# Performance work log

Hardware: AMD Instinct MI355X
Metric: run time of the kernel (lower is better)

The kernel has to match this reference:

```python
import jax, jax.numpy as jnp
import numpy as np
from jax import lax

D = 512
K = 5
HID = 2 * D
EPS = 1e-5


def layernorm(x, g, b):
    mu = jnp.mean(x, axis=-1, keepdims=True)
    var = jnp.mean((x - mu) ** 2, axis=-1, keepdims=True)
    return (x - mu) * lax.rsqrt(var + EPS) * g + b


def setup_inputs() -> dict:
    key = jax.random.key(0)
    ks = jax.random.split(key, 16)
    B, T = 8, 4096
    sc = lambda fan: 1.0 / np.sqrt(fan)
    return {
        "x": jax.random.normal(ks[0], (B, T, D), jnp.float32),
        "decay_logit": jnp.zeros((D,), jnp.float32),
        "W_out": jax.random.uniform(ks[1], (D, D), jnp.float32, -sc(D), sc(D)),
        "b_out": jax.random.uniform(ks[2], (D,), jnp.float32, -sc(D), sc(D)),
        "conv_w": jax.random.uniform(ks[3], (D, 1, K), jnp.float32, -sc(K), sc(K)),
        "conv_b": jax.random.uniform(ks[4], (D,), jnp.float32, -sc(K), sc(K)),
        "ln1_g": jnp.ones((D,), jnp.float32),
        "ln1_b": jnp.zeros((D,), jnp.float32),
        "ln2_g": jnp.ones((D,), jnp.float32),
        "ln2_b": jnp.zeros((D,), jnp.float32),
        "W1": jax.random.uniform(ks[5], (HID, D), jnp.float32, -sc(D), sc(D)),
        "b1": jax.random.uniform(ks[6], (HID,), jnp.float32, -sc(D), sc(D)),
        "W2": jax.random.uniform(ks[7], (D, HID), jnp.float32, -sc(HID), sc(HID)),
        "b2": jax.random.uniform(ks[8], (D,), jnp.float32, -sc(HID), sc(HID)),
    }


def retention_core(xn, decay_logit, W_out, b_out, conv_w, conv_b):
    # xn: [B, T, D]
    B, T, _ = xn.shape
    a = jax.nn.sigmoid(decay_logit)  # [D]

    def step(s, xt):  # s, xt: [B, D]
        s = a * s + (1.0 - a) * xt
        return s, s

    s0 = jnp.zeros((B, D), xn.dtype)
    _, ss = lax.scan(step, s0, jnp.swapaxes(xn, 0, 1))  # [T, B, D]
    ss = jnp.swapaxes(ss, 0, 1)  # [B, T, D]
    y_ret = jnp.einsum("btd,ed->bte", ss, W_out) + b_out

    # depthwise conv1d, 'same' padding (K odd)
    xc = jnp.swapaxes(xn, 1, 2)  # [B, D, T]
    pad = (K - 1) // 2
    y_loc = lax.conv_general_dilated(
        xc, conv_w, window_strides=(1,), padding=[(pad, pad)],
        feature_group_count=D, dimension_numbers=("NCH", "OIH", "NCH"))
    y_loc = jnp.swapaxes(y_loc + conv_b[None, :, None], 1, 2)  # [B, T, D]
    return y_ret + y_loc


def reference(x, decay_logit, W_out, b_out, conv_w, conv_b,
              ln1_g, ln1_b, ln2_g, ln2_b, W1, b1, W2, b2):
    y = retention_core(layernorm(x, ln1_g, ln1_b),
                       decay_logit, W_out, b_out, conv_w, conv_b)
    x = x + y
    h = layernorm(x, ln2_g, ln2_b)
    h = jax.nn.gelu(jnp.einsum("btd,hd->bth", h, W1) + b1, approximate=False)
    y = jnp.einsum("bth,dh->btd", h, W2) + b2
    return x + y
```

## Files before the change

kernel.cpp:

```cpp
#include <hip/hip_runtime.h>
#include <stdint.h>

typedef unsigned short u16;

#define DIM 512
#define HIDN 1024
#define TT 4096
#define BB 8
#define MM 32768
#define CH 128
#define CL 32

__device__ __forceinline__ u16 f2bf(float f) {
  union { float f; uint32_t u; } v; v.f = f;
  uint32_t u = v.u;
  uint32_t r = u + 0x7fffu + ((u >> 16) & 1u);
  return (u16)(r >> 16);
}
__device__ __forceinline__ float bf2f(u16 h) {
  union { uint32_t u; float f; } v; v.u = ((uint32_t)h) << 16; return v.f;
}

typedef __bf16 bf16x8 __attribute__((ext_vector_type(8)));
typedef float f32x4 __attribute__((ext_vector_type(4)));

__global__ __launch_bounds__(256) void prep_kernel(
    const float* __restrict__ wout, const float* __restrict__ w1,
    const float* __restrict__ w2, const float* __restrict__ dl,
    const float* __restrict__ convw,
    u16* __restrict__ wout_h, u16* __restrict__ w1_h, u16* __restrict__ w2_h,
    float* __restrict__ a, float* __restrict__ oma, float* __restrict__ aL,
    float* __restrict__ convwT) {
  int i = blockIdx.x * 256 + threadIdx.x;
  if (i < DIM * DIM) wout_h[i] = f2bf(wout[i]);
  if (i < HIDN * DIM) { w1_h[i] = f2bf(w1[i]); w2_h[i] = f2bf(w2[i]); }
  if (i < 5 * DIM) {
    int kk = i / DIM, n = i - kk * DIM;
    convwT[i] = convw[n * 5 + kk];
  }
  if (i < DIM) {
    float av = 1.0f / (1.0f + expf(-dl[i]));
    a[i] = av; oma[i] = 1.0f - av; aL[i] = powf(av, (float)CL);
  }
}

__global__ __launch_bounds__(256) void ln_rows(
    const float* __restrict__ xin, const float* __restrict__ g,
    const float* __restrict__ bvec, u16* __restrict__ out) {
  int lane = threadIdx.x & 63, wave = threadIdx.x >> 6;
  size_t row = (size_t)blockIdx.x * 4 + wave;
  const float4* xr = (const float4*)(xin + row * DIM);
  float4 v0 = xr[lane * 2 + 0];
  float4 v1 = xr[lane * 2 + 1];
  float s1 = v0.x + v0.y + v0.z + v0.w + v1.x + v1.y + v1.z + v1.w;
  float s2 = v0.x * v0.x + v0.y * v0.y + v0.z * v0.z + v0.w * v0.w
           + v1.x * v1.x + v1.y * v1.y + v1.z * v1.z + v1.w * v1.w;
#pragma unroll
  for (int o = 1; o < 64; o <<= 1) { s1 += __shfl_xor(s1, o); s2 += __shfl_xor(s2, o); }
  float mu = s1 * (1.0f / DIM);
  float var = s2 * (1.0f / DIM) - mu * mu;
  float rs = rsqrtf(var + 1e-5f);
  const float4* gr = (const float4*)g;
  const float4* br = (const float4*)bvec;
  float4 g0 = gr[lane * 2], g1 = gr[lane * 2 + 1];
  float4 b0 = br[lane * 2], b1 = br[lane * 2 + 1];
  uint32_t p0 = (uint32_t)f2bf((v0.x - mu) * rs * g0.x + b0.x) | ((uint32_t)f2bf((v0.y - mu) * rs * g0.y + b0.y) << 16);
  uint32_t p1 = (uint32_t)f2bf((v0.z - mu) * rs * g0.z + b0.z) | ((uint32_t)f2bf((v0.w - mu) * rs * g0.w + b0.w) << 16);
  uint32_t p2 = (uint32_t)f2bf((v1.x - mu) * rs * g1.x + b1.x) | ((uint32_t)f2bf((v1.y - mu) * rs * g1.y + b1.y) << 16);
  uint32_t p3 = (uint32_t)f2bf((v1.z - mu) * rs * g1.z + b1.z) | ((uint32_t)f2bf((v1.w - mu) * rs * g1.w + b1.w) << 16);
  uint4 pk; pk.x = p0; pk.y = p1; pk.z = p2; pk.w = p3;
  ((uint4*)(out + row * DIM))[lane] = pk;
}

__global__ __launch_bounds__(256) void scan_local(
    const u16* __restrict__ xn, const float* __restrict__ a,
    const float* __restrict__ oma, float* __restrict__ carry) {
  int idx = blockIdx.x * 256 + threadIdx.x;
  int dp = (idx & 255) * 2;
  int c = (idx >> 8) & (CH - 1);
  int b = idx >> 15;
  float a0 = a[dp], a1 = a[dp + 1], o0 = oma[dp], o1 = oma[dp + 1];
  const uint32_t* xp = (const uint32_t*)(xn + ((size_t)(b * TT + c * CL)) * DIM + dp);
  float s0 = 0.f, s1 = 0.f;
#pragma unroll
  for (int i = 0; i < CL; ++i) {
    uint32_t u = xp[(size_t)i * (DIM / 2)];
    s0 = fmaf(a0, s0, o0 * bf2f((u16)(u & 0xffffu)));
    s1 = fmaf(a1, s1, o1 * bf2f((u16)(u >> 16)));
  }
  float2 cv; cv.x = s0; cv.y = s1;
  *(float2*)&carry[((size_t)(b * CH + c)) * DIM + dp] = cv;
}

__global__ __launch_bounds__(256) void scan_carry(
    const float* __restrict__ carry, const float* __restrict__ aL,
    float* __restrict__ start) {
  int idx = blockIdx.x * 256 + threadIdx.x;
  int d = idx & (DIM - 1);
  int b = idx >> 9;
  float al = aL[d];
  float s = 0.f;
#pragma unroll 8
  for (int c = 0; c < CH; ++c) {
    size_t o = ((size_t)(b * CH + c)) * DIM + d;
    start[o] = s;
    s = fmaf(al, s, carry[o]);
  }
}

__global__ __launch_bounds__(256) void scan_emit(
    const u16* __restrict__ xn, const float* __restrict__ a,
    const float* __restrict__ oma, const float* __restrict__ start,
    u16* __restrict__ ss) {
  int idx = blockIdx.x * 256 + threadIdx.x;
  int dp = (idx & 255) * 2;
  int c = (idx >> 8) & (CH - 1);
  int b = idx >> 15;
  float a0 = a[dp], a1 = a[dp + 1], o0 = oma[dp], o1 = oma[dp + 1];
  const uint32_t* xp = (const uint32_t*)(xn + ((size_t)(b * TT + c * CL)) * DIM + dp);
  uint32_t* sp = (uint32_t*)(ss + ((size_t)(b * TT + c * CL)) * DIM + dp);
  float2 st = *(const float2*)&start[((size_t)(b * CH + c)) * DIM + dp];
  float s0 = st.x, s1 = st.y;
#pragma unroll
  for (int i = 0; i < CL; ++i) {
    uint32_t u = xp[(size_t)i * (DIM / 2)];
    s0 = fmaf(a0, s0, o0 * bf2f((u16)(u & 0xffffu)));
    s1 = fmaf(a1, s1, o1 * bf2f((u16)(u >> 16)));
    sp[(size_t)i * (DIM / 2)] = (uint32_t)f2bf(s0) | ((uint32_t)f2bf(s1) << 16);
  }
}

template <int Kd, int NCOL, int EPI>
__global__ __launch_bounds__(512, 4) void gemm_bt(
    const u16* __restrict__ A, const u16* __restrict__ Bmat,
    const float* __restrict__ bias, const float* __restrict__ resid,
    const u16* __restrict__ xn, const float* __restrict__ convwT,
    const float* __restrict__ convb, float* __restrict__ outf,
    u16* __restrict__ outh) {
  __shared__ alignas(16) u16 sA[2][128 * 64];
  __shared__ alignas(16) u16 sB[2][128 * 64];
  const int tid = threadIdx.x;
  const int lane = tid & 63, wave = tid >> 6;
  const int wm = wave >> 2;
  const int wn = wave & 3;
  const int rA = lane & 15, q = lane >> 4;

  const int lin = blockIdx.x;
  const int tile_col = (lin >> 3) & (NCOL - 1);
  const int tile_row = (lin & 7) + 8 * ((lin >> 3) / NCOL);
  const size_t rowTile = (size_t)tile_row * 128;
  const size_t colTile = (size_t)tile_col * 128;

  f32x4 acc[4][2];
#pragma unroll
  for (int i = 0; i < 4; i++)
#pragma unroll
    for (int j = 0; j < 2; j++) acc[i][j] = (f32x4){0.f, 0.f, 0.f, 0.f};

  const u16* Abase = A + rowTile * Kd;
  const u16* Bbase = Bmat + colTile * Kd;

  const int lrow = lane >> 3;
  const int lslot = lane & 7;
  const int gk = ((lslot ^ lrow) & 7) * 8;

  auto stage = [&](int kt, int buf) {
#pragma unroll
    for (int it = 0; it < 2; ++it) {
      const int m0 = (it * 8 + wave) * 8;
      const u16* ga = Abase + (size_t)(m0 + lrow) * Kd + kt + gk;
      const u16* gb = Bbase + (size_t)(m0 + lrow) * Kd + kt + gk;
      __builtin_amdgcn_global_load_lds(
          (const __attribute__((address_space(1))) void*)ga,
          (__attribute__((address_space(3))) void*)&sA[buf][m0 * 64], 16, 0, 0);
      __builtin_amdgcn_global_load_lds(
          (const __attribute__((address_space(1))) void*)gb,
          (__attribute__((address_space(3))) void*)&sB[buf][m0 * 64], 16, 0, 0);
    }
  };

  constexpr int NI = Kd / 64;
  stage(0, 0);
#pragma unroll 1
  for (int i = 0; i < NI; ++i) {
    __asm__ __volatile__("s_barrier" ::: "memory");
    if (i + 1 < NI) {
      stage((i + 1) * 64, (i + 1) & 1);
      __asm__ __volatile__("s_waitcnt vmcnt(4)" ::: "memory");
    } else {
      __asm__ __volatile__("s_waitcnt vmcnt(0)" ::: "memory");
    }
    __asm__ __volatile__("s_barrier" ::: "memory");
    const u16* bufA = sA[i & 1];
    const u16* bufB = sB[i & 1];
#pragma unroll
    for (int ks = 0; ks < 2; ++ks) {
      bf16x8 af[4], bfr[2];
#pragma unroll
      for (int mi = 0; mi < 4; ++mi) {
        int r = wm * 64 + mi * 16 + rA;
        int pos = ((ks * 4 + q) ^ (r & 7));
        af[mi] = *(const bf16x8*)&bufA[r * 64 + pos * 8];
      }
#pragma unroll
      for (int ni = 0; ni < 2; ++ni) {
        int r = wn * 32 + ni * 16 + rA;
        int pos = ((ks * 4 + q) ^ (r & 7));
        bfr[ni] = *(const bf16x8*)&bufB[r * 64 + pos * 8];
      }
#pragma unroll
      for (int mi = 0; mi < 4; ++mi)
#pragma unroll
        for (int ni = 0; ni < 2; ++ni)
          acc[mi][ni] = __builtin_amdgcn_mfma_f32_16x16x32_bf16(bfr[ni], af[mi], acc[mi][ni], 0, 0, 0);
    }
  }

#pragma unroll
  for (int mi = 0; mi < 4; ++mi) {
    size_t m = rowTile + wm * 64 + mi * 16 + rA;
#pragma unroll
    for (int ni = 0; ni < 2; ++ni) {
      int n0 = (int)colTile + wn * 32 + ni * 16 + q * 4;
      f32x4 v = acc[mi][ni];
      float4 bv = *(const float4*)&bias[n0];
      float val0 = v[0] + bv.x, val1 = v[1] + bv.y, val2 = v[2] + bv.z, val3 = v[3] + bv.w;
      if constexpr (EPI == 0) {
        int t = (int)(m & (TT - 1));
        float4 cb = *(const float4*)&convb[n0];
        float4 rv = *(const float4*)&resid[m * DIM + n0];
        val0 += cb.x + rv.x; val1 += cb.y + rv.y; val2 += cb.z + rv.z; val3 += cb.w + rv.w;
#pragma unroll
        for (int kk = 0; kk < 5; ++kk) {
          int ttc = t + kk - 2;
          if (ttc >= 0 && ttc < TT) {
            uint2 xv = *(const uint2*)&xn[(m + (size_t)kk - 2) * DIM + n0];
            float4 wv = *(const float4*)&convwT[kk * DIM + n0];
            val0 = fmaf(wv.x, bf2f((u16)(xv.x & 0xffffu)), val0);
            val1 = fmaf(wv.y, bf2f((u16)(xv.x >> 16)), val1);
            val2 = fmaf(wv.z, bf2f((u16)(xv.y & 0xffffu)), val2);
            val3 = fmaf(wv.w, bf2f((u16)(xv.y >> 16)), val3);
          }
        }
        float4 ov; ov.x = val0; ov.y = val1; ov.z = val2; ov.w = val3;
        *(float4*)&outf[m * DIM + n0] = ov;
      } else if constexpr (EPI == 1) {
        const float isq2 = 0.70710678118654752f;
        float g0 = 0.5f * val0 * (1.0f + erff(val0 * isq2));
        float g1 = 0.5f * val1 * (1.0f + erff(val1 * isq2));
        float g2 = 0.5f * val2 * (1.0f + erff(val2 * isq2));
        float g3 = 0.5f * val3 * (1.0f + erff(val3 * isq2));
        uint2 pk;
        pk.x = (uint32_t)f2bf(g0) | ((uint32_t)f2bf(g1) << 16);
        pk.y = (uint32_t)f2bf(g2) | ((uint32_t)f2bf(g3) << 16);
        *(uint2*)&outh[m * HIDN + n0] = pk;
      } else {
        float4 rv = *(const float4*)&resid[m * DIM + n0];
        float4 ov;
        ov.x = val0 + rv.x; ov.y = val1 + rv.y; ov.z = val2 + rv.z; ov.w = val3 + rv.w;
        *(float4*)&outf[m * DIM + n0] = ov;
      }
    }
  }
}

extern "C" void kernel_launch(void* const* d_in, const int* in_sizes, int n_in,
                              void* d_out, int out_size, void* d_ws, size_t ws_size,
                              hipStream_t stream) {
  const float* x      = (const float*)d_in[0];
  const float* dl     = (const float*)d_in[1];
  const float* W_out  = (const float*)d_in[2];
  const float* b_out  = (const float*)d_in[3];
  const float* conv_w = (const float*)d_in[4];
  const float* conv_b = (const float*)d_in[5];
  const float* ln1_g  = (const float*)d_in[6];
  const float* ln1_b  = (const float*)d_in[7];
  const float* ln2_g  = (const float*)d_in[8];
  const float* ln2_b  = (const float*)d_in[9];
  const float* W1     = (const float*)d_in[10];
  const float* b1     = (const float*)d_in[11];
  const float* W2     = (const float*)d_in[12];
  const float* b2     = (const float*)d_in[13];

  char* ws = (char*)d_ws;
  u16*   wout_h = (u16*)(ws + 0);
  u16*   w1_h   = (u16*)(ws + 524288);
  u16*   w2_h   = (u16*)(ws + 1572864);
  float* a_buf  = (float*)(ws + 2621440);
  float* oma    = (float*)(ws + 2623488);
  float* aL     = (float*)(ws + 2625536);
  float* convwT = (float*)(ws + 2627584);
  float* carry  = (float*)(ws + (4u << 20));
  float* start  = (float*)(ws + 6291456);
  u16*   xn  = (u16*)(ws + (8u << 20));
  u16*   ssb = (u16*)(ws + (40u << 20));
  float* x1  = (float*)(ws + (72u << 20));
  u16*   h   = (u16*)(ws + (136u << 20));
  u16*   hg  = (u16*)(ws + (168u << 20));

  float* out = (float*)d_out;

  prep_kernel<<<2048, 256, 0, stream>>>(W_out, W1, W2, dl, conv_w, wout_h, w1_h, w2_h, a_buf, oma, aL, convwT);
  ln_rows<<<MM / 4, 256, 0, stream>>>(x, ln1_g, ln1_b, xn);
  scan_local<<<(BB * CH * DIM / 2) / 256, 256, 0, stream>>>(xn, a_buf, oma, carry);
  scan_carry<<<(BB * DIM) / 256, 256, 0, stream>>>(carry, aL, start);
  scan_emit<<<(BB * CH * DIM / 2) / 256, 256, 0, stream>>>(xn, a_buf, oma, start, ssb);
  gemm_bt<512, 4, 0><<<1024, 512, 0, stream>>>(ssb, wout_h, b_out, x, xn, convwT, conv_b, x1, nullptr);
  ln_rows<<<MM / 4, 256, 0, stream>>>(x1, ln2_g, ln2_b, h);
  gemm_bt<512, 8, 1><<<2048, 512, 0, stream>>>(h, w1_h, b1, nullptr, nullptr, nullptr, nullptr, nullptr, hg);
  gemm_bt<1024, 4, 2><<<1024, 512, 0, stream>>>(hg, w2_h, b2, x1, nullptr, nullptr, nullptr, out, nullptr);
}
```

Measured before the change: 376.4 us.

## Fuse second LayerNorm into output-projection GEMM with full-row tiles

Replaces the W_out GEMM plus separate ln_rows pass with one kernel whose blocks each own 64 full rows (all 512 columns). Row sums and sums of squares are reduced across lanes and waves through LDS, and the normalized bf16 activations are written directly. This removes a kernel launch and the re-read of x1 for the second LayerNorm. In exchange it uses 1024-thread blocks with about 148 KB of LDS, which limits occupancy to one block per CU. It also computes variance as E[x^2]-mu^2, which is less numerically robust.

```diff
diff --git a/kernel.cpp b/kernel.cpp
--- a/kernel.cpp
+++ b/kernel.cpp
@@ -130,13 +130,176 @@
   }
 }
 
+__global__ __launch_bounds__(1024, 4) void gemm1_ln(
+    const u16* __restrict__ A, const u16* __restrict__ Bmat,
+    const float* __restrict__ bias, const float* __restrict__ resid,
+    const u16* __restrict__ xn, const float* __restrict__ convwT,
+    const float* __restrict__ convb, const float* __restrict__ lng,
+    const float* __restrict__ lnb, float* __restrict__ outf,
+    u16* __restrict__ outh) {
+  extern __shared__ __align__(16) u16 lds[];
+  float2* stats2 = (float2*)(lds + 73728);
+  const int tid = threadIdx.x;
+  const int lane = tid & 63, wave = tid >> 6;
+  const int wm = wave >> 3;
+  const int wn = wave & 7;
+  const int rA = lane & 15, q = lane >> 4;
+
+  const size_t rowTile = (size_t)blockIdx.x * 64;
+
+  f32x4 acc[2][4];
+#pragma unroll
+  for (int i = 0; i < 2; i++)
+#pragma unroll
+    for (int j = 0; j < 4; j++) acc[i][j] = (f32x4){0.f, 0.f, 0.f, 0.f};
+
+  const u16* Abase = A + rowTile * DIM;
+  const u16* Bbase = Bmat;
+
+  const int lrow = lane >> 3;
+  const int lslot = lane & 7;
+  const int gk = ((lslot ^ lrow) & 7) * 8;
+
+  auto stage = [&](int kt, int buf) {
+#pragma unroll
+    for (int it = 0; it < 4; ++it) {
+      const int g = it * 16 + wave;
+      const u16* gb = Bbase + (size_t)(g * 8 + lrow) * DIM + kt + gk;
+      __builtin_amdgcn_global_load_lds(
+          (const __attribute__((address_space(1))) void*)gb,
+          (__attribute__((address_space(3))) void*)(lds + 8192 + buf * 32768 + g * 512), 16, 0, 0);
+    }
+    if (wave < 8) {
+      const int g = wave;
+      const u16* ga = Abase + (size_t)(g * 8 + lrow) * DIM + kt + gk;
+      __builtin_amdgcn_global_load_lds(
+          (const __attribute__((address_space(1))) void*)ga,
+          (__attribute__((address_space(3))) void*)(lds + buf * 4096 + g * 512), 16, 0, 0);
+    }
+  };
+
+  constexpr int NI = DIM / 64;
+  stage(0, 0);
+#pragma unroll 1
+  for (int i = 0; i < NI; ++i) {
+    __asm__ __volatile__("s_barrier" ::: "memory");
+    if (i + 1 < NI) {
+      stage((i + 1) * 64, (i + 1) & 1);
+      if (wave < 8) { __asm__ __volatile__("s_waitcnt vmcnt(5)" ::: "memory"); }
+      else          { __asm__ __volatile__("s_waitcnt vmcnt(4)" ::: "memory"); }
+    } else {
+      __asm__ __volatile__("s_waitcnt vmcnt(0)" ::: "memory");
+    }
+    __asm__ __volatile__("s_barrier" ::: "memory");
+    const u16* bufA = lds + (i & 1) * 4096;
+    const u16* bufB = lds + 8192 + (i & 1) * 32768;
+#pragma unroll
+    for (int ks = 0; ks < 2; ++ks) {
+      bf16x8 af[2], bfr[4];
+#pragma unroll
+      for (int mi = 0; mi < 2; ++mi) {
+        int r = wm * 32 + mi * 16 + rA;
+        int pos = ((ks * 4 + q) ^ (r & 7));
+        af[mi] = *(const bf16x8*)&bufA[r * 64 + pos * 8];
+      }
+#pragma unroll
+      for (int ni = 0; ni < 4; ++ni) {
+        int r = wn * 64 + ni * 16 + rA;
+        int pos = ((ks * 4 + q) ^ (r & 7));
+        bfr[ni] = *(const bf16x8*)&bufB[r * 64 + pos * 8];
+      }
+#pragma unroll
+      for (int mi = 0; mi < 2; ++mi)
+#pragma unroll
+        for (int ni = 0; ni < 4; ++ni)
+          acc[mi][ni] = __builtin_amdgcn_mfma_f32_16x16x32_bf16(bfr[ni], af[mi], acc[mi][ni], 0, 0, 0);
+    }
+  }
+
+  float val[2][4][4];
+  float s1w[2], s2w[2];
+#pragma unroll
+  for (int mi = 0; mi < 2; ++mi) {
+    size_t m = rowTile + wm * 32 + mi * 16 + rA;
+    int t = (int)(m & (TT - 1));
+    float s1 = 0.f, s2 = 0.f;
+#pragma unroll
+    for (int ni = 0; ni < 4; ++ni) {
+      int n0 = wn * 64 + ni * 16 + q * 4;
+      f32x4 v = acc[mi][ni];
+      float4 bv = *(const float4*)&bias[n0];
+      float4 cb = *(const float4*)&convb[n0];
+      float4 rv = *(const float4*)&resid[m * DIM + n0];
+      float v0 = v[0] + bv.x + cb.x + rv.x;
+      float v1 = v[1] + bv.y + cb.y + rv.y;
+      float v2 = v[2] + bv.z + cb.z + rv.z;
+      float v3 = v[3] + bv.w + cb.w + rv.w;
+#pragma unroll
+      for (int kk = 0; kk < 5; ++kk) {
+        int ttc = t + kk - 2;
+        if (ttc >= 0 && ttc < TT) {
+          uint2 xv = *(const uint2*)&xn[(m + (size_t)kk - 2) * DIM + n0];
+          float4 wv = *(const float4*)&convwT[kk * DIM + n0];
+          v0 = fmaf(wv.x, bf2f((u16)(xv.x & 0xffffu)), v0);
+          v1 = fmaf(wv.y, bf2f((u16)(xv.x >> 16)), v1);
+          v2 = fmaf(wv.z, bf2f((u16)(xv.y & 0xffffu)), v2);
+          v3 = fmaf(wv.w, bf2f((u16)(xv.y >> 16)), v3);
+        }
+      }
+      val[mi][ni][0] = v0; val[mi][ni][1] = v1; val[mi][ni][2] = v2; val[mi][ni][3] = v3;
+      float4 ov; ov.x = v0; ov.y = v1; ov.z = v2; ov.w = v3;
+      *(float4*)&outf[m * DIM + n0] = ov;
+      s1 += v0 + v1 + v2 + v3;
+      s2 += v0 * v0 + v1 * v1 + v2 * v2 + v3 * v3;
+    }
+    s1 += __shfl_xor(s1, 16); s1 += __shfl_xor(s1, 32);
+    s2 += __shfl_xor(s2, 16); s2 += __shfl_xor(s2, 32);
+    s1w[mi] = s1; s2w[mi] = s2;
+  }
+  if (q == 0) {
+#pragma unroll
+    for (int mi = 0; mi < 2; ++mi) {
+      int row = wm * 32 + mi * 16 + rA;
+      float2 st; st.x = s1w[mi]; st.y = s2w[mi];
+      stats2[row * 8 + wn] = st;
+    }
+  }
+  __syncthreads();
+#pragma unroll
+  for (int mi = 0; mi < 2; ++mi) {
+    int row = wm * 32 + mi * 16 + rA;
+    size_t m = rowTile + row;
+    float s1 = 0.f, s2 = 0.f;
+#pragma unroll
+    for (int w = 0; w < 8; ++w) {
+      float2 st = stats2[row * 8 + w];
+      s1 += st.x; s2 += st.y;
+    }
+    float mu = s1 * (1.0f / DIM);
+    float var = s2 * (1.0f / DIM) - mu * mu;
+    float rs = rsqrtf(var + 1e-5f);
+#pragma unroll
+    for (int ni = 0; ni < 4; ++ni) {
+      int n0 = wn * 64 + ni * 16 + q * 4;
+      float4 gv = *(const float4*)&lng[n0];
+      float4 bv = *(const float4*)&lnb[n0];
+      float h0 = (val[mi][ni][0] - mu) * rs * gv.x + bv.x;
+      float h1 = (val[mi][ni][1] - mu) * rs * gv.y + bv.y;
+      float h2 = (val[mi][ni][2] - mu) * rs * gv.z + bv.z;
+      float h3 = (val[mi][ni][3] - mu) * rs * gv.w + bv.w;
+      uint2 pk;
+      pk.x = (uint32_t)f2bf(h0) | ((uint32_t)f2bf(h1) << 16);
+      pk.y = (uint32_t)f2bf(h2) | ((uint32_t)f2bf(h3) << 16);
+      *(uint2*)&outh[m * DIM + n0] = pk;
+    }
+  }
+}
+
 template <int Kd, int NCOL, int EPI>
 __global__ __launch_bounds__(512, 4) void gemm_bt(
     const u16* __restrict__ A, const u16* __restrict__ Bmat,
     const float* __restrict__ bias, const float* __restrict__ resid,
-    const u16* __restrict__ xn, const float* __restrict__ convwT,
-    const float* __restrict__ convb, float* __restrict__ outf,
-    u16* __restrict__ outh) {
+    float* __restrict__ outf, u16* __restrict__ outh) {
   __shared__ alignas(16) u16 sA[2][128 * 64];
   __shared__ alignas(16) u16 sB[2][128 * 64];
   const int tid = threadIdx.x;
@@ -225,26 +388,7 @@
       f32x4 v = acc[mi][ni];
       float4 bv = *(const float4*)&bias[n0];
       float val0 = v[0] + bv.x, val1 = v[1] + bv.y, val2 = v[2] + bv.z, val3 = v[3] + bv.w;
-      if constexpr (EPI == 0) {
-        int t = (int)(m & (TT - 1));
-        float4 cb = *(const float4*)&convb[n0];
-        float4 rv = *(const float4*)&resid[m * DIM + n0];
-        val0 += cb.x + rv.x; val1 += cb.y + rv.y; val2 += cb.z + rv.z; val3 += cb.w + rv.w;
-#pragma unroll
-        for (int kk = 0; kk < 5; ++kk) {
-          int ttc = t + kk - 2;
-          if (ttc >= 0 && ttc < TT) {
-            uint2 xv = *(const uint2*)&xn[(m + (size_t)kk - 2) * DIM + n0];
-            float4 wv = *(const float4*)&convwT[kk * DIM + n0];
-            val0 = fmaf(wv.x, bf2f((u16)(xv.x & 0xffffu)), val0);
-            val1 = fmaf(wv.y, bf2f((u16)(xv.x >> 16)), val1);
-            val2 = fmaf(wv.z, bf2f((u16)(xv.y & 0xffffu)), val2);
-            val3 = fmaf(wv.w, bf2f((u16)(xv.y >> 16)), val3);
-          }
-        }
-        float4 ov; ov.x = val0; ov.y = val1; ov.z = val2; ov.w = val3;
-        *(float4*)&outf[m * DIM + n0] = ov;
-      } else if constexpr (EPI == 1) {
+      if constexpr (EPI == 1) {
         const float isq2 = 0.70710678118654752f;
         float g0 = 0.5f * val0 * (1.0f + erff(val0 * isq2));
         float g1 = 0.5f * val1 * (1.0f + erff(val1 * isq2));
@@ -300,13 +444,15 @@
 
   float* out = (float*)d_out;
 
+  hipFuncSetAttribute(reinterpret_cast<const void*>(&gemm1_ln),
+                      hipFuncAttributeMaxDynamicSharedMemorySize, 151552);
+
   prep_kernel<<<2048, 256, 0, stream>>>(W_out, W1, W2, dl, conv_w, wout_h, w1_h, w2_h, a_buf, oma, aL, convwT);
   ln_rows<<<MM / 4, 256, 0, stream>>>(x, ln1_g, ln1_b, xn);
   scan_local<<<(BB * CH * DIM / 2) / 256, 256, 0, stream>>>(xn, a_buf, oma, carry);
   scan_carry<<<(BB * DIM) / 256, 256, 0, stream>>>(carry, aL, start);
   scan_emit<<<(BB * CH * DIM / 2) / 256, 256, 0, stream>>>(xn, a_buf, oma, start, ssb);
-  gemm_bt<512, 4, 0><<<1024, 512, 0, stream>>>(ssb, wout_h, b_out, x, xn, convwT, conv_b, x1, nullptr);
-  ln_rows<<<MM / 4, 256, 0, stream>>>(x1, ln2_g, ln2_b, h);
-  gemm_bt<512, 8, 1><<<2048, 512, 0, stream>>>(h, w1_h, b1, nullptr, nullptr, nullptr, nullptr, nullptr, hg);
-  gemm_bt<1024, 4, 2><<<1024, 512, 0, stream>>>(hg, w2_h, b2, x1, nullptr, nullptr, nullptr, out, nullptr);
-}
+  gemm1_ln<<<MM / 64, 1024, 151552, stream>>>(ssb, wout_h, b_out, x, xn, convwT, conv_b, ln2_g, ln2_b, x1, h);
+  gemm_bt<512, 8, 1><<<2048, 512, 0, stream>>>(h, w1_h, b1, nullptr, nullptr, hg);
+  gemm_bt<1024, 4, 2><<<1024, 512, 0, stream>>>(hg, w2_h, b2, x1, out, nullptr);
+}
```

After: 388.6 us. +3.3%, slower.
